# Kernel tuning notes

Hardware: AMD Instinct MI355X
Metric: run time of the kernel (lower is better)

## Reference

```python
import jax, jax.numpy as jnp
import numpy as np

# Static graph / model sizes (closed over; match input_specs)
N0, N1, N2 = 500_000, 100_000, 25_000   # nodes per hop (targets are prefix of sources)
E0, E1 = 1_600_000, 400_000             # edges per hop
D_IN, D_H, D_OUT = 128, 256, 128


def setup_inputs() -> dict:
    key = jax.random.key(0)
    ks = jax.random.split(key, 11)
    s_in = 1.0 / np.sqrt(D_IN)
    s_h = 1.0 / np.sqrt(D_H)
    return {
        "x": jax.random.normal(ks[0], (N0, D_IN), dtype=jnp.float32),
        # layer 0 params (SAGEConv in->hidden): lin_l (with bias) on aggregated, lin_r (no bias) on root
        "W_l0": jax.random.normal(ks[1], (D_H, D_IN), dtype=jnp.float32) * s_in,
        "b_l0": jax.random.normal(ks[2], (D_H,), dtype=jnp.float32) * s_in,
        "W_r0": jax.random.normal(ks[3], (D_H, D_IN), dtype=jnp.float32) * s_in,
        # layer 1 params (SAGEConv hidden->out)
        "W_l1": jax.random.normal(ks[4], (D_OUT, D_H), dtype=jnp.float32) * s_h,
        "b_l1": jax.random.normal(ks[5], (D_OUT,), dtype=jnp.float32) * s_h,
        "W_r1": jax.random.normal(ks[6], (D_OUT, D_H), dtype=jnp.float32) * s_h,
        # bipartite edge indices: src in [0, N_src), dst in [0, N_dst)
        "ei0_src": jax.random.randint(ks[7], (E0,), 0, N0),
        "ei0_dst": jax.random.randint(ks[8], (E0,), 0, N1),
        "ei1_src": jax.random.randint(ks[9], (E1,), 0, N1),
        "ei1_dst": jax.random.randint(ks[10], (E1,), 0, N2),
    }


def _sage_conv(x_src, x_dst, src, dst, n_dst, W_l, b_l, W_r):
    """PyG SAGEConv, aggr='mean': lin_l(mean_neigh) + lin_r(x_dst)."""
    msg = x_src[src]                                                # [E, d] gather
    agg = jax.ops.segment_sum(msg, dst, num_segments=n_dst)        # [n_dst, d]
    cnt = jax.ops.segment_sum(jnp.ones((src.shape[0],), msg.dtype), dst,
                              num_segments=n_dst)                  # [n_dst]
    agg = agg / jnp.clip(cnt, 1.0)[:, None]                        # mean (safe for isolated nodes)
    return agg @ W_l.T + b_l + x_dst @ W_r.T


def reference(x, W_l0, b_l0, W_r0, W_l1, b_l1, W_r1,
              ei0_src, ei0_dst, ei1_src, ei1_dst):
    # hop 0: targets are first N1 rows of x
    h = _sage_conv(x, x[:N1], ei0_src, ei0_dst, N1, W_l0, b_l0, W_r0)
    h = jax.nn.relu(h)  # relu on all but last layer
    # hop 1 (last layer, no relu)
    out = _sage_conv(h, h[:N2], ei1_src, ei1_dst, N2, W_l1, b_l1, W_r1)
    return out
```

## Files before the change

kernel.cpp:

```cpp
#include <hip/hip_runtime.h>
#include <hip/hip_bf16.h>

#define cN0 500000
#define cN1 100000
#define cN2 25000
#define cE0 1600000
#define cE1 400000

typedef __bf16 bf16x8 __attribute__((ext_vector_type(8)));
typedef __bf16 bf16x4 __attribute__((ext_vector_type(4)));
typedef float f32x4 __attribute__((ext_vector_type(4)));


__global__ void k_hist(const int* __restrict__ dst, int E, int* __restrict__ cnt) {
    int i = blockIdx.x * blockDim.x + threadIdx.x;
    if (i < E) atomicAdd(&cnt[dst[i]], 1);
}

__global__ void k_scan1(int* __restrict__ a, int n, int* __restrict__ bsum) {
    __shared__ int lds[256];
    const int t = threadIdx.x;
    const int base = blockIdx.x * 1024 + t * 4;
    int v0 = (base + 0 < n) ? a[base + 0] : 0;
    int v1 = (base + 1 < n) ? a[base + 1] : 0;
    int v2 = (base + 2 < n) ? a[base + 2] : 0;
    int v3 = (base + 3 < n) ? a[base + 3] : 0;
    const int s = v0 + v1 + v2 + v3;
    lds[t] = s;
    __syncthreads();
    int x = s;
    for (int d = 1; d < 256; d <<= 1) {
        int y = (t >= d) ? lds[t - d] : 0;
        __syncthreads();
        x += y;
        lds[t] = x;
        __syncthreads();
    }
    if (t == 255) bsum[blockIdx.x] = x;
    int e0 = x - s;
    int e1 = e0 + v0, e2 = e1 + v1, e3 = e2 + v2;
    if (base + 0 < n) a[base + 0] = e0;
    if (base + 1 < n) a[base + 1] = e1;
    if (base + 2 < n) a[base + 2] = e2;
    if (base + 3 < n) a[base + 3] = e3;
}

__global__ void k_scan2(int* __restrict__ bsum, int nb) {
    __shared__ int lds[128];
    const int t = threadIdx.x;
    int v = (t < nb) ? bsum[t] : 0;
    lds[t] = v;
    __syncthreads();
    int x = v;
    for (int d = 1; d < 128; d <<= 1) {
        int y = (t >= d) ? lds[t - d] : 0;
        __syncthreads();
        x += y;
        lds[t] = x;
        __syncthreads();
    }
    if (t < nb) bsum[t] = x - v;
}

__global__ void k_scan3(int* __restrict__ a, int n, const int* __restrict__ bsum, int total) {
    int i = blockIdx.x * blockDim.x + threadIdx.x;
    if (i < n) a[i] += bsum[i >> 10];
    if (i == 0) a[n] = total;
}

__global__ void k_copy(int* __restrict__ dst, const int* __restrict__ src, int n) {
    int i = blockIdx.x * blockDim.x + threadIdx.x;
    if (i < n) dst[i] = src[i];
}

__global__ void k_scatter(const int* __restrict__ esrc, const int* __restrict__ edst, int E,
                          int* __restrict__ cur, int* __restrict__ srcs) {
    int i = blockIdx.x * blockDim.x + threadIdx.x;
    if (i < E) {
        int p = atomicAdd(&cur[edst[i]], 1);
        srcs[p] = esrc[i];
    }
}

__global__ void k_wcat0(const float* __restrict__ Wl, const float* __restrict__ Wr,
                        __bf16* __restrict__ Wc) {
    int i = blockIdx.x * blockDim.x + threadIdx.x;
    if (i < 256 * 256) {
        int j = i >> 8, k = i & 255;
        float v = (k < 128) ? Wl[j * 128 + k] : Wr[j * 128 + (k - 128)];
        Wc[i] = (__bf16)v;
    }
}
__global__ void k_wcat1(const float* __restrict__ Wl, const float* __restrict__ Wr,
                        __bf16* __restrict__ Wc) {
    int i = blockIdx.x * blockDim.x + threadIdx.x;
    if (i < 128 * 512) {
        int j = i >> 9, k = i & 511;
        float v = (k < 256) ? Wl[j * 256 + k] : Wr[j * 256 + (k - 256)];
        Wc[i] = (__bf16)v;
    }
}

__global__ __launch_bounds__(256) void k_agg0(
    const float* __restrict__ x,
    const int* __restrict__ off, const int* __restrict__ srcs,
    __bf16* __restrict__ M0)
{
    const int tid = threadIdx.x;
    const int slot = tid >> 5;
    const int ln = tid & 31;
    const int g = blockIdx.x * 8 + slot;
    if (g >= cN1) return;
    const int e0 = off[g], e1 = off[g + 1];
    float ax = 0.f, ay = 0.f, az = 0.f, aw = 0.f;
    int e = e0;
    for (; e + 4 <= e1; e += 4) {
        const int s0 = srcs[e], s1 = srcs[e + 1], s2 = srcs[e + 2], s3 = srcs[e + 3];
        const float4 r0 = *(const float4*)(x + (size_t)s0 * 128 + ln * 4);
        const float4 r1 = *(const float4*)(x + (size_t)s1 * 128 + ln * 4);
        const float4 r2 = *(const float4*)(x + (size_t)s2 * 128 + ln * 4);
        const float4 r3 = *(const float4*)(x + (size_t)s3 * 128 + ln * 4);
        ax += (r0.x + r1.x) + (r2.x + r3.x);
        ay += (r0.y + r1.y) + (r2.y + r3.y);
        az += (r0.z + r1.z) + (r2.z + r3.z);
        aw += (r0.w + r1.w) + (r2.w + r3.w);
    }
    for (; e < e1; ++e) {
        const int s = srcs[e];
        const float4 r = *(const float4*)(x + (size_t)s * 128 + ln * 4);
        ax += r.x; ay += r.y; az += r.z; aw += r.w;
    }
    const int cnt = e1 - e0;
    const float inv = 1.f / (float)(cnt > 0 ? cnt : 1);
    bf16x4 oa;
    oa[0] = (__bf16)(ax * inv); oa[1] = (__bf16)(ay * inv);
    oa[2] = (__bf16)(az * inv); oa[3] = (__bf16)(aw * inv);
    *(bf16x4*)(M0 + (size_t)g * 256 + ln * 4) = oa;
    const float4 xd = *(const float4*)(x + (size_t)g * 128 + ln * 4);
    bf16x4 ox;
    ox[0] = (__bf16)xd.x; ox[1] = (__bf16)xd.y;
    ox[2] = (__bf16)xd.z; ox[3] = (__bf16)xd.w;
    *(bf16x4*)(M0 + (size_t)g * 256 + 128 + ln * 4) = ox;
}

__global__ __launch_bounds__(256) void k_agg1(
    const __bf16* __restrict__ h,
    const int* __restrict__ off, const int* __restrict__ srcs,
    __bf16* __restrict__ M1)
{
    const int tid = threadIdx.x;
    const int wave = tid >> 6;
    const int lane = tid & 63;
    const int g = blockIdx.x * 4 + wave;
    if (g >= cN2) return;
    const int e0 = off[g], e1 = off[g + 1];
    float a0 = 0.f, a1 = 0.f, a2 = 0.f, a3 = 0.f;
    int e = e0;
    for (; e + 4 <= e1; e += 4) {
        const int s0 = srcs[e], s1 = srcs[e + 1], s2 = srcs[e + 2], s3 = srcs[e + 3];
        const bf16x4 r0 = *(const bf16x4*)(h + (size_t)s0 * 256 + lane * 4);
        const bf16x4 r1 = *(const bf16x4*)(h + (size_t)s1 * 256 + lane * 4);
        const bf16x4 r2 = *(const bf16x4*)(h + (size_t)s2 * 256 + lane * 4);
        const bf16x4 r3 = *(const bf16x4*)(h + (size_t)s3 * 256 + lane * 4);
        a0 += (float)r0[0] + (float)r1[0] + (float)r2[0] + (float)r3[0];
        a1 += (float)r0[1] + (float)r1[1] + (float)r2[1] + (float)r3[1];
        a2 += (float)r0[2] + (float)r1[2] + (float)r2[2] + (float)r3[2];
        a3 += (float)r0[3] + (float)r1[3] + (float)r2[3] + (float)r3[3];
    }
    for (; e < e1; ++e) {
        const int s = srcs[e];
        const bf16x4 r = *(const bf16x4*)(h + (size_t)s * 256 + lane * 4);
        a0 += (float)r[0]; a1 += (float)r[1]; a2 += (float)r[2]; a3 += (float)r[3];
    }
    const int cnt = e1 - e0;
    const float inv = 1.f / (float)(cnt > 0 ? cnt : 1);
    bf16x4 oa;
    oa[0] = (__bf16)(a0 * inv); oa[1] = (__bf16)(a1 * inv);
    oa[2] = (__bf16)(a2 * inv); oa[3] = (__bf16)(a3 * inv);
    *(bf16x4*)(M1 + (size_t)g * 512 + lane * 4) = oa;
    *(bf16x4*)(M1 + (size_t)g * 512 + 256 + lane * 4) =
        *(const bf16x4*)(h + (size_t)g * 256 + lane * 4);
}

template<int K, int LDC, bool RELU, bool OUTBF16>
__global__ __launch_bounds__(256) void k_gemm(
    const __bf16* __restrict__ Mm, const __bf16* __restrict__ W,
    const float* __restrict__ bias,
    float* __restrict__ outf, __bf16* __restrict__ outb, int Mrows)
{
    const int tid = threadIdx.x;
    const int l = tid & 63;
    const int w = tid >> 6;
    const int wm = w & 1, wn = w >> 1;
    const int row0 = blockIdx.x * 128 + wm * 64;
    const int col0 = blockIdx.y * 128 + wn * 64;
    const int lr = l & 15;
    const int lk = (l >> 4) * 8;

    const __bf16* pa[4];
    const __bf16* pb[4];
    #pragma unroll
    for (int i = 0; i < 4; ++i) {
        int r = row0 + i * 16 + lr;
        r = (r < Mrows) ? r : (Mrows - 1);
        pa[i] = Mm + (size_t)r * K + lk;
        pb[i] = W + (size_t)(col0 + i * 16 + lr) * K + lk;
    }
    f32x4 acc[4][4];
    #pragma unroll
    for (int i = 0; i < 4; ++i)
        #pragma unroll
        for (int j = 0; j < 4; ++j)
            acc[i][j] = (f32x4)0.0f;

    #pragma unroll 2
    for (int k0 = 0; k0 < K; k0 += 32) {
        bf16x8 fa[4], fb[4];
        #pragma unroll
        for (int i = 0; i < 4; ++i) fa[i] = *(const bf16x8*)(pa[i] + k0);
        #pragma unroll
        for (int j = 0; j < 4; ++j) fb[j] = *(const bf16x8*)(pb[j] + k0);
        #pragma unroll
        for (int i = 0; i < 4; ++i)
            #pragma unroll
            for (int j = 0; j < 4; ++j)
                acc[i][j] = __builtin_amdgcn_mfma_f32_16x16x32_bf16(fa[i], fb[j], acc[i][j], 0, 0, 0);
    }

    #pragma unroll
    for (int j = 0; j < 4; ++j) {
        const int colg = col0 + j * 16 + lr;
        const float bj = bias[colg];
        #pragma unroll
        for (int i = 0; i < 4; ++i) {
            #pragma unroll
            for (int reg = 0; reg < 4; ++reg) {
                const int rowg = row0 + i * 16 + (l >> 4) * 4 + reg;
                if (rowg < Mrows) {
                    float v = acc[i][j][reg] + bj;
                    if (RELU) v = fmaxf(v, 0.f);
                    if (OUTBF16) outb[(size_t)rowg * LDC + colg] = (__bf16)v;
                    else         outf[(size_t)rowg * LDC + colg] = v;
                }
            }
        }
    }
}


extern "C" void kernel_launch(void* const* d_in, const int* in_sizes, int n_in,
                              void* d_out, int out_size, void* d_ws, size_t ws_size,
                              hipStream_t stream) {
    const float* x   = (const float*)d_in[0];
    const float* Wl0 = (const float*)d_in[1];
    const float* bl0 = (const float*)d_in[2];
    const float* Wr0 = (const float*)d_in[3];
    const float* Wl1 = (const float*)d_in[4];
    const float* bl1 = (const float*)d_in[5];
    const float* Wr1 = (const float*)d_in[6];
    const int* e0s = (const int*)d_in[7];
    const int* e0d = (const int*)d_in[8];
    const int* e1s = (const int*)d_in[9];
    const int* e1d = (const int*)d_in[10];
    float* out = (float*)d_out;

    char* ws = (char*)d_ws;
    size_t pos = 0;
    auto alloc = [&](size_t nb) -> void* {
        void* p = ws + pos;
        pos += (nb + 255) & ~(size_t)255;
        return p;
    };
    __bf16* M0   = (__bf16*)alloc((size_t)cN1 * 256 * 2);
    __bf16* M1   = M0;
    __bf16* h    = (__bf16*)alloc((size_t)cN1 * 256 * 2);
    int* off0    = (int*)alloc((size_t)(cN1 + 1) * 4);
    int* cur0    = (int*)alloc((size_t)cN1 * 4);
    int* srcs0   = (int*)alloc((size_t)cE0 * 4);
    int* off1    = (int*)alloc((size_t)(cN2 + 1) * 4);
    int* cur1    = (int*)alloc((size_t)cN2 * 4);
    int* srcs1   = (int*)alloc((size_t)cE1 * 4);
    int* bsum    = (int*)alloc(128 * 4);
    __bf16* Wc0  = (__bf16*)alloc(256 * 256 * 2);
    __bf16* Wc1  = (__bf16*)alloc(128 * 512 * 2);
    (void)ws_size; (void)in_sizes; (void)n_in; (void)out_size;

    hipMemsetAsync(off0, 0, (size_t)(cN1 + 1) * 4, stream);
    hipMemsetAsync(off1, 0, (size_t)(cN2 + 1) * 4, stream);
    k_hist<<<(cE0 + 255) / 256, 256, 0, stream>>>(e0d, cE0, off0);
    k_hist<<<(cE1 + 255) / 256, 256, 0, stream>>>(e1d, cE1, off1);

    const int nb0 = (cN1 + 1023) / 1024;
    k_scan1<<<nb0, 256, 0, stream>>>(off0, cN1, bsum);
    k_scan2<<<1, 128, 0, stream>>>(bsum, nb0);
    k_scan3<<<(cN1 + 255) / 256, 256, 0, stream>>>(off0, cN1, bsum, cE0);
    k_copy<<<(cN1 + 255) / 256, 256, 0, stream>>>(cur0, off0, cN1);
    k_scatter<<<(cE0 + 255) / 256, 256, 0, stream>>>(e0s, e0d, cE0, cur0, srcs0);

    const int nb1 = (cN2 + 1023) / 1024;
    k_scan1<<<nb1, 256, 0, stream>>>(off1, cN2, bsum);
    k_scan2<<<1, 128, 0, stream>>>(bsum, nb1);
    k_scan3<<<(cN2 + 255) / 256, 256, 0, stream>>>(off1, cN2, bsum, cE1);
    k_copy<<<(cN2 + 255) / 256, 256, 0, stream>>>(cur1, off1, cN2);
    k_scatter<<<(cE1 + 255) / 256, 256, 0, stream>>>(e1s, e1d, cE1, cur1, srcs1);

    k_wcat0<<<(256 * 256 + 255) / 256, 256, 0, stream>>>(Wl0, Wr0, Wc0);
    k_wcat1<<<(128 * 512 + 255) / 256, 256, 0, stream>>>(Wl1, Wr1, Wc1);

    k_agg0<<<(cN1 + 7) / 8, 256, 0, stream>>>(x, off0, srcs0, M0);
    {
        dim3 grid((cN1 + 127) / 128, 2);
        k_gemm<256, 256, true, true><<<grid, 256, 0, stream>>>(M0, Wc0, bl0, nullptr, h, cN1);
    }
    k_agg1<<<(cN2 + 3) / 4, 256, 0, stream>>>(h, off1, srcs1, M1);
    {
        dim3 grid((cN2 + 127) / 128, 1);
        k_gemm<512, 128, false, false><<<grid, 256, 0, stream>>>(M1, Wc1, bl1, out, nullptr, cN2);
    }
}
```

Measured before the change: 829.6 us.

## Pre-cast features to bf16, split GEMM A operand, and restructure gather kernels

New measurement: 879.4 us. 6.0% more time.

```diff
diff --git a/kernel.cpp b/kernel.cpp
--- a/kernel.cpp
+++ b/kernel.cpp
@@ -62,15 +62,15 @@
     if (t < nb) bsum[t] = x - v;
 }
 
-__global__ void k_scan3(int* __restrict__ a, int n, const int* __restrict__ bsum, int total) {
-    int i = blockIdx.x * blockDim.x + threadIdx.x;
-    if (i < n) a[i] += bsum[i >> 10];
+__global__ void k_scan3(int* __restrict__ a, int n, const int* __restrict__ bsum, int total,
+                        int* __restrict__ cur) {
+    int i = blockIdx.x * blockDim.x + threadIdx.x;
+    if (i < n) {
+        int v = a[i] + bsum[i >> 10];
+        a[i] = v;
+        cur[i] = v;
+    }
     if (i == 0) a[n] = total;
-}
-
-__global__ void k_copy(int* __restrict__ dst, const int* __restrict__ src, int n) {
-    int i = blockIdx.x * blockDim.x + threadIdx.x;
-    if (i < n) dst[i] = src[i];
 }
 
 __global__ void k_scatter(const int* __restrict__ esrc, const int* __restrict__ edst, int E,
@@ -79,6 +79,19 @@
     if (i < E) {
         int p = atomicAdd(&cur[edst[i]], 1);
         srcs[p] = esrc[i];
+    }
+}
+
+__global__ __launch_bounds__(256) void k_cast(const float* __restrict__ x,
+                                              __bf16* __restrict__ xb, int n8) {
+    int i = blockIdx.x * blockDim.x + threadIdx.x;
+    if (i < n8) {
+        const float4 v0 = *(const float4*)(x + (size_t)i * 8);
+        const float4 v1 = *(const float4*)(x + (size_t)i * 8 + 4);
+        bf16x8 o;
+        o[0] = (__bf16)v0.x; o[1] = (__bf16)v0.y; o[2] = (__bf16)v0.z; o[3] = (__bf16)v0.w;
+        o[4] = (__bf16)v1.x; o[5] = (__bf16)v1.y; o[6] = (__bf16)v1.z; o[7] = (__bf16)v1.w;
+        *(bf16x8*)(xb + (size_t)i * 8) = o;
     }
 }
 
@@ -102,92 +115,91 @@
 }
 
 __global__ __launch_bounds__(256) void k_agg0(
-    const float* __restrict__ x,
+    const __bf16* __restrict__ xb,
     const int* __restrict__ off, const int* __restrict__ srcs,
-    __bf16* __restrict__ M0)
+    const __bf16* __restrict__ zrow,
+    __bf16* __restrict__ Agg)
 {
-    const int tid = threadIdx.x;
-    const int slot = tid >> 5;
-    const int ln = tid & 31;
-    const int g = blockIdx.x * 8 + slot;
-    if (g >= cN1) return;
-    const int e0 = off[g], e1 = off[g + 1];
-    float ax = 0.f, ay = 0.f, az = 0.f, aw = 0.f;
-    int e = e0;
-    for (; e + 4 <= e1; e += 4) {
-        const int s0 = srcs[e], s1 = srcs[e + 1], s2 = srcs[e + 2], s3 = srcs[e + 3];
-        const float4 r0 = *(const float4*)(x + (size_t)s0 * 128 + ln * 4);
-        const float4 r1 = *(const float4*)(x + (size_t)s1 * 128 + ln * 4);
-        const float4 r2 = *(const float4*)(x + (size_t)s2 * 128 + ln * 4);
-        const float4 r3 = *(const float4*)(x + (size_t)s3 * 128 + ln * 4);
-        ax += (r0.x + r1.x) + (r2.x + r3.x);
-        ay += (r0.y + r1.y) + (r2.y + r3.y);
-        az += (r0.z + r1.z) + (r2.z + r3.z);
-        aw += (r0.w + r1.w) + (r2.w + r3.w);
-    }
-    for (; e < e1; ++e) {
-        const int s = srcs[e];
-        const float4 r = *(const float4*)(x + (size_t)s * 128 + ln * 4);
-        ax += r.x; ay += r.y; az += r.z; aw += r.w;
-    }
-    const int cnt = e1 - e0;
-    const float inv = 1.f / (float)(cnt > 0 ? cnt : 1);
-    bf16x4 oa;
-    oa[0] = (__bf16)(ax * inv); oa[1] = (__bf16)(ay * inv);
-    oa[2] = (__bf16)(az * inv); oa[3] = (__bf16)(aw * inv);
-    *(bf16x4*)(M0 + (size_t)g * 256 + ln * 4) = oa;
-    const float4 xd = *(const float4*)(x + (size_t)g * 128 + ln * 4);
-    bf16x4 ox;
-    ox[0] = (__bf16)xd.x; ox[1] = (__bf16)xd.y;
-    ox[2] = (__bf16)xd.z; ox[3] = (__bf16)xd.w;
-    *(bf16x4*)(M0 + (size_t)g * 256 + 128 + ln * 4) = ox;
+    const int wid = blockIdx.x * 4 + (threadIdx.x >> 6);
+    const int lane = threadIdx.x & 63;
+    const int slot = lane >> 4;
+    const int dl = lane & 15;
+    const int gbase = wid * 8;
+    for (int n = 0; n < 8; ++n) {
+        const int g = gbase + n;
+        if (g >= cN1) return;
+        const int e0 = off[g], e1 = off[g + 1];
+        const int deg = e1 - e0;
+        float a[8] = {0.f, 0.f, 0.f, 0.f, 0.f, 0.f, 0.f, 0.f};
+        const int iters = (deg + 3) >> 2;
+        for (int it = 0; it < iters; ++it) {
+            const int e = e0 + it * 4 + slot;
+            const __bf16* rp = zrow;
+            if (e < e1) rp = xb + (size_t)srcs[e] * 128;
+            const bf16x8 r = *(const bf16x8*)(rp + dl * 8);
+            #pragma unroll
+            for (int d = 0; d < 8; ++d) a[d] += (float)r[d];
+        }
+        #pragma unroll
+        for (int d = 0; d < 8; ++d) {
+            a[d] += __shfl_xor(a[d], 16);
+            a[d] += __shfl_xor(a[d], 32);
+        }
+        if (slot == 0) {
+            const float inv = 1.f / (float)(deg > 0 ? deg : 1);
+            bf16x8 o;
+            #pragma unroll
+            for (int d = 0; d < 8; ++d) o[d] = (__bf16)(a[d] * inv);
+            *(bf16x8*)(Agg + (size_t)g * 128 + dl * 8) = o;
+        }
+    }
 }
 
 __global__ __launch_bounds__(256) void k_agg1(
     const __bf16* __restrict__ h,
     const int* __restrict__ off, const int* __restrict__ srcs,
-    __bf16* __restrict__ M1)
+    const __bf16* __restrict__ zrow,
+    __bf16* __restrict__ Agg)
 {
-    const int tid = threadIdx.x;
-    const int wave = tid >> 6;
-    const int lane = tid & 63;
-    const int g = blockIdx.x * 4 + wave;
-    if (g >= cN2) return;
-    const int e0 = off[g], e1 = off[g + 1];
-    float a0 = 0.f, a1 = 0.f, a2 = 0.f, a3 = 0.f;
-    int e = e0;
-    for (; e + 4 <= e1; e += 4) {
-        const int s0 = srcs[e], s1 = srcs[e + 1], s2 = srcs[e + 2], s3 = srcs[e + 3];
-        const bf16x4 r0 = *(const bf16x4*)(h + (size_t)s0 * 256 + lane * 4);
-        const bf16x4 r1 = *(const bf16x4*)(h + (size_t)s1 * 256 + lane * 4);
-        const bf16x4 r2 = *(const bf16x4*)(h + (size_t)s2 * 256 + lane * 4);
-        const bf16x4 r3 = *(const bf16x4*)(h + (size_t)s3 * 256 + lane * 4);
-        a0 += (float)r0[0] + (float)r1[0] + (float)r2[0] + (float)r3[0];
-        a1 += (float)r0[1] + (float)r1[1] + (float)r2[1] + (float)r3[1];
-        a2 += (float)r0[2] + (float)r1[2] + (float)r2[2] + (float)r3[2];
-        a3 += (float)r0[3] + (float)r1[3] + (float)r2[3] + (float)r3[3];
-    }
-    for (; e < e1; ++e) {
-        const int s = srcs[e];
-        const bf16x4 r = *(const bf16x4*)(h + (size_t)s * 256 + lane * 4);
-        a0 += (float)r[0]; a1 += (float)r[1]; a2 += (float)r[2]; a3 += (float)r[3];
-    }
-    const int cnt = e1 - e0;
-    const float inv = 1.f / (float)(cnt > 0 ? cnt : 1);
-    bf16x4 oa;
-    oa[0] = (__bf16)(a0 * inv); oa[1] = (__bf16)(a1 * inv);
-    oa[2] = (__bf16)(a2 * inv); oa[3] = (__bf16)(a3 * inv);
-    *(bf16x4*)(M1 + (size_t)g * 512 + lane * 4) = oa;
-    *(bf16x4*)(M1 + (size_t)g * 512 + 256 + lane * 4) =
-        *(const bf16x4*)(h + (size_t)g * 256 + lane * 4);
-}
-
-template<int K, int LDC, bool RELU, bool OUTBF16>
+    const int wid = blockIdx.x * 4 + (threadIdx.x >> 6);
+    const int lane = threadIdx.x & 63;
+    const int slot = lane >> 5;
+    const int dl = lane & 31;
+    const int gbase = wid * 4;
+    for (int n = 0; n < 4; ++n) {
+        const int g = gbase + n;
+        if (g >= cN2) return;
+        const int e0 = off[g], e1 = off[g + 1];
+        const int deg = e1 - e0;
+        float a[8] = {0.f, 0.f, 0.f, 0.f, 0.f, 0.f, 0.f, 0.f};
+        const int iters = (deg + 1) >> 1;
+        for (int it = 0; it < iters; ++it) {
+            const int e = e0 + it * 2 + slot;
+            const __bf16* rp = zrow;
+            if (e < e1) rp = h + (size_t)srcs[e] * 256;
+            const bf16x8 r = *(const bf16x8*)(rp + dl * 8);
+            #pragma unroll
+            for (int d = 0; d < 8; ++d) a[d] += (float)r[d];
+        }
+        #pragma unroll
+        for (int d = 0; d < 8; ++d) a[d] += __shfl_xor(a[d], 32);
+        if (slot == 0) {
+            const float inv = 1.f / (float)(deg > 0 ? deg : 1);
+            bf16x8 o;
+            #pragma unroll
+            for (int d = 0; d < 8; ++d) o[d] = (__bf16)(a[d] * inv);
+            *(bf16x8*)(Agg + (size_t)g * 256 + dl * 8) = o;
+        }
+    }
+}
+
+template<int KHALF, int LDC, bool RELU, bool OUTBF16>
 __global__ __launch_bounds__(256) void k_gemm(
-    const __bf16* __restrict__ Mm, const __bf16* __restrict__ W,
-    const float* __restrict__ bias,
+    const __bf16* __restrict__ A1, const __bf16* __restrict__ A2,
+    const __bf16* __restrict__ W, const float* __restrict__ bias,
     float* __restrict__ outf, __bf16* __restrict__ outb, int Mrows)
 {
+    const int K = KHALF * 2;
     const int tid = threadIdx.x;
     const int l = tid & 63;
     const int w = tid >> 6;
@@ -197,13 +209,15 @@
     const int lr = l & 15;
     const int lk = (l >> 4) * 8;
 
-    const __bf16* pa[4];
+    const __bf16* pa1[4];
+    const __bf16* pa2[4];
     const __bf16* pb[4];
     #pragma unroll
     for (int i = 0; i < 4; ++i) {
         int r = row0 + i * 16 + lr;
         r = (r < Mrows) ? r : (Mrows - 1);
-        pa[i] = Mm + (size_t)r * K + lk;
+        pa1[i] = A1 + (size_t)r * KHALF + lk;
+        pa2[i] = A2 + (size_t)r * KHALF + lk;
         pb[i] = W + (size_t)(col0 + i * 16 + lr) * K + lk;
     }
     f32x4 acc[4][4];
@@ -214,12 +228,25 @@
             acc[i][j] = (f32x4)0.0f;
 
     #pragma unroll 2
-    for (int k0 = 0; k0 < K; k0 += 32) {
+    for (int k0 = 0; k0 < KHALF; k0 += 32) {
         bf16x8 fa[4], fb[4];
         #pragma unroll
-        for (int i = 0; i < 4; ++i) fa[i] = *(const bf16x8*)(pa[i] + k0);
+        for (int i = 0; i < 4; ++i) fa[i] = *(const bf16x8*)(pa1[i] + k0);
         #pragma unroll
         for (int j = 0; j < 4; ++j) fb[j] = *(const bf16x8*)(pb[j] + k0);
+        #pragma unroll
+        for (int i = 0; i < 4; ++i)
+            #pragma unroll
+            for (int j = 0; j < 4; ++j)
+                acc[i][j] = __builtin_amdgcn_mfma_f32_16x16x32_bf16(fa[i], fb[j], acc[i][j], 0, 0, 0);
+    }
+    #pragma unroll 2
+    for (int k0 = 0; k0 < KHALF; k0 += 32) {
+        bf16x8 fa[4], fb[4];
+        #pragma unroll
+        for (int i = 0; i < 4; ++i) fa[i] = *(const bf16x8*)(pa2[i] + k0);
+        #pragma unroll
+        for (int j = 0; j < 4; ++j) fb[j] = *(const bf16x8*)(pb[j] + KHALF + k0);
         #pragma unroll
         for (int i = 0; i < 4; ++i)
             #pragma unroll
@@ -271,9 +298,10 @@
         pos += (nb + 255) & ~(size_t)255;
         return p;
     };
-    __bf16* M0   = (__bf16*)alloc((size_t)cN1 * 256 * 2);
-    __bf16* M1   = M0;
+    __bf16* xb   = (__bf16*)alloc((size_t)cN0 * 128 * 2);
     __bf16* h    = (__bf16*)alloc((size_t)cN1 * 256 * 2);
+    __bf16* Agg0 = (__bf16*)alloc((size_t)cN1 * 128 * 2);
+    __bf16* Agg1 = Agg0;
     int* off0    = (int*)alloc((size_t)(cN1 + 1) * 4);
     int* cur0    = (int*)alloc((size_t)cN1 * 4);
     int* srcs0   = (int*)alloc((size_t)cE0 * 4);
@@ -283,38 +311,40 @@
     int* bsum    = (int*)alloc(128 * 4);
     __bf16* Wc0  = (__bf16*)alloc(256 * 256 * 2);
     __bf16* Wc1  = (__bf16*)alloc(128 * 512 * 2);
+    __bf16* zrow = (__bf16*)alloc(256 * 2);
     (void)ws_size; (void)in_sizes; (void)n_in; (void)out_size;
 
     hipMemsetAsync(off0, 0, (size_t)(cN1 + 1) * 4, stream);
     hipMemsetAsync(off1, 0, (size_t)(cN2 + 1) * 4, stream);
+    hipMemsetAsync(zrow, 0, 256 * 2, stream);
+    k_cast<<<(cN0 * 128 / 8 + 255) / 256, 256, 0, stream>>>(x, xb, cN0 * 128 / 8);
+
     k_hist<<<(cE0 + 255) / 256, 256, 0, stream>>>(e0d, cE0, off0);
     k_hist<<<(cE1 + 255) / 256, 256, 0, stream>>>(e1d, cE1, off1);
 
     const int nb0 = (cN1 + 1023) / 1024;
     k_scan1<<<nb0, 256, 0, stream>>>(off0, cN1, bsum);
     k_scan2<<<1, 128, 0, stream>>>(bsum, nb0);
-    k_scan3<<<(cN1 + 255) / 256, 256, 0, stream>>>(off0, cN1, bsum, cE0);
-    k_copy<<<(cN1 + 255) / 256, 256, 0, stream>>>(cur0, off0, cN1);
+    k_scan3<<<(cN1 + 255) / 256, 256, 0, stream>>>(off0, cN1, bsum, cE0, cur0);
     k_scatter<<<(cE0 + 255) / 256, 256, 0, stream>>>(e0s, e0d, cE0, cur0, srcs0);
 
     const int nb1 = (cN2 + 1023) / 1024;
     k_scan1<<<nb1, 256, 0, stream>>>(off1, cN2, bsum);
     k_scan2<<<1, 128, 0, stream>>>(bsum, nb1);
-    k_scan3<<<(cN2 + 255) / 256, 256, 0, stream>>>(off1, cN2, bsum, cE1);
-    k_copy<<<(cN2 + 255) / 256, 256, 0, stream>>>(cur1, off1, cN2);
+    k_scan3<<<(cN2 + 255) / 256, 256, 0, stream>>>(off1, cN2, bsum, cE1, cur1);
     k_scatter<<<(cE1 + 255) / 256, 256, 0, stream>>>(e1s, e1d, cE1, cur1, srcs1);
 
     k_wcat0<<<(256 * 256 + 255) / 256, 256, 0, stream>>>(Wl0, Wr0, Wc0);
     k_wcat1<<<(128 * 512 + 255) / 256, 256, 0, stream>>>(Wl1, Wr1, Wc1);
 
-    k_agg0<<<(cN1 + 7) / 8, 256, 0, stream>>>(x, off0, srcs0, M0);
+    k_agg0<<<(cN1 + 31) / 32, 256, 0, stream>>>(xb, off0, srcs0, zrow, Agg0);
     {
         dim3 grid((cN1 + 127) / 128, 2);
-        k_gemm<256, 256, true, true><<<grid, 256, 0, stream>>>(M0, Wc0, bl0, nullptr, h, cN1);
-    }
-    k_agg1<<<(cN2 + 3) / 4, 256, 0, stream>>>(h, off1, srcs1, M1);
+        k_gemm<128, 256, true, true><<<grid, 256, 0, stream>>>(Agg0, xb, Wc0, bl0, nullptr, h, cN1);
+    }
+    k_agg1<<<(cN2 + 15) / 16, 256, 0, stream>>>(h, off1, srcs1, zrow, Agg1);
     {
         dim3 grid((cN2 + 127) / 128, 1);
-        k_gemm<512, 128, false, false><<<grid, 256, 0, stream>>>(M1, Wc1, bl1, out, nullptr, cN2);
-    }
-}
+        k_gemm<256, 128, false, false><<<grid, 256, 0, stream>>>(Agg1, h, Wc1, bl1, out, nullptr, cN2);
+    }
+}
```
